# Kernel tuning notes

Hardware: AMD Instinct MI355X
Metric: run time of the kernel (lower is better)

The kernel has to match this reference:

```python
import jax, jax.numpy as jnp
import numpy as np

B, S, D, F_DIM, E, TOP_K = 4, 2048, 1024, 1024, 8, 2


def setup_inputs() -> dict:
    key = jax.random.key(0)
    ks = jax.random.split(key, 6)
    return {
        "x": jax.random.normal(ks[0], (B, S, D), jnp.float32),
        "router_w": jax.random.normal(ks[1], (E, D), jnp.float32) * 0.02,
        "router_b": jax.random.normal(ks[2], (E,), jnp.float32) * 0.02,
        "expert_w": jax.random.normal(ks[3], (E, F_DIM, D), jnp.float32) * 0.02,
        "expert_b": jax.random.normal(ks[4], (E, F_DIM), jnp.float32) * 0.02,
        "expert_pref": jax.random.normal(ks[5], (E, D), jnp.float32),
        "top_k": TOP_K,
    }


def reference(x, router_w, router_b, expert_w, expert_b, expert_pref, top_k):
    num_experts = expert_w.shape[0]
    # Router: softmax over experts, then top-k with renormalization
    logits = jnp.einsum("bsd,ed->bse", x, router_w) + router_b
    routing_weights = jax.nn.softmax(logits, axis=-1)            # [B,S,E]
    top_w, top_idx = jax.lax.top_k(routing_weights, top_k)       # [B,S,K]
    top_w = top_w / jnp.sum(top_w, axis=-1, keepdims=True)
    # Dense per-expert combine weight: sum of renormalized top-k weights routed to each expert
    onehot = jax.nn.one_hot(top_idx, num_experts, dtype=x.dtype)  # [B,S,K,E]
    comb = jnp.einsum("bske,bsk->bse", onehot, top_w)             # [B,S,E]
    # Per-expert linear for every token, weighted combine (dense grouped-GEMM form)
    expert_out = jnp.einsum("bsd,efd->bsef", x, expert_w) + expert_b  # [B,S,E,F]
    final_output = jnp.einsum("bsef,bse->bsf", expert_out, comb)      # [B,S,F]
    # Expert utilization: fraction of tokens whose top-k contains expert i
    mask = jnp.sum(onehot, axis=2) > 0                            # [B,S,E]
    expert_utilization = jnp.mean(mask.astype(x.dtype), axis=(0, 1))
    # Load balance loss: MSE of mean routing weight vs ideal uniform usage
    usage = jnp.mean(routing_weights, axis=(0, 1))
    load_balance_loss = jnp.mean((usage - 1.0 / num_experts) ** 2)
    # Diversity: mean pairwise L2 distance over concatenated expert params (fixed small E)
    flat = jnp.concatenate(
        [expert_w.reshape(num_experts, -1), expert_b, expert_pref], axis=1
    )  # [E, P]
    dists = [jnp.linalg.norm(flat[i] - flat[j])
             for i in range(num_experts) for j in range(i + 1, num_experts)]
    diversity_score = jnp.mean(jnp.stack(dists))
    return final_output, routing_weights, expert_utilization, load_balance_loss, diversity_score
```

## Files before the change

kernel.cpp:

```cpp
#include <hip/hip_runtime.h>
#include <stdint.h>

typedef unsigned short u16;
typedef __attribute__((ext_vector_type(4))) float f32x4;
typedef __attribute__((ext_vector_type(8))) short bf16x8;

#define NTOK 8192
#define DDIM 1024
#define FDIM 1024
#define NEXP 8
#define PCAP 8192
#define RBLK 512

__device__ __align__(256) u16 g_xb[NTOK * DDIM];
__device__ __align__(256) u16 g_wbf[NEXP * FDIM * DDIM];
__device__ __align__(256) float g_buf0[NTOK * FDIM];
__device__ __align__(256) float g_buf1[NTOK * FDIM];
__device__ __align__(256) int g_ptok[NEXP * PCAP];
__device__ __align__(256) float g_pw[NEXP * PCAP];
__device__ __align__(256) unsigned g_e01[NTOK];
__device__ __align__(256) float g_w0[NTOK];
__device__ __align__(256) float g_w1[NTOK];
__device__ __align__(256) float g_usage_part[RBLK * NEXP];
__device__ __align__(256) int g_tile[256];
__device__ int g_ntile;
__device__ int g_cnt[16];
__device__ float g_gram[40];

__device__ __forceinline__ u16 f2bf(float f) {
  unsigned u = __builtin_bit_cast(unsigned, f);
  unsigned r = u + 0x7fffu + ((u >> 16) & 1u);
  return (u16)(r >> 16);
}

__device__ __forceinline__ void gload_lds16(const void* g, void* l) {
  __builtin_amdgcn_global_load_lds(
      (const __attribute__((address_space(1))) void*)g,
      (__attribute__((address_space(3))) void*)l, 16, 0, 0);
}

__global__ __launch_bounds__(64) void k_init() {
  const int tid = threadIdx.x;
  if (tid < 40) g_gram[tid] = 0.f;
}

__global__ __launch_bounds__(256) void k_gram_cast(
    const float* __restrict__ ew, const float* __restrict__ ebias,
    const float* __restrict__ epref) {
  const int P0 = FDIM * DDIM;
  const int PT = P0 + FDIM + DDIM;
  float g[36];
#pragma unroll
  for (int i = 0; i < 36; ++i) g[i] = 0.f;
  for (int k = blockIdx.x * 256 + threadIdx.x; k < PT; k += gridDim.x * 256) {
    float v[8];
    if (k < P0) {
#pragma unroll
      for (int e = 0; e < 8; ++e) v[e] = ew[(size_t)e * P0 + k];
#pragma unroll
      for (int e = 0; e < 8; ++e) g_wbf[(size_t)e * P0 + k] = f2bf(v[e]);
    } else if (k < P0 + FDIM) {
      int kk = k - P0;
#pragma unroll
      for (int e = 0; e < 8; ++e) v[e] = ebias[e * FDIM + kk];
    } else {
      int kk = k - P0 - FDIM;
#pragma unroll
      for (int e = 0; e < 8; ++e) v[e] = epref[e * DDIM + kk];
    }
    int idx = 0;
#pragma unroll
    for (int i = 0; i < 8; ++i)
#pragma unroll
      for (int j = i; j < 8; ++j) {
        g[idx] += v[i] * v[j];
        ++idx;
      }
  }
#pragma unroll
  for (int i = 0; i < 36; ++i) {
    float a = g[i];
#pragma unroll
    for (int s = 32; s; s >>= 1) a += __shfl_xor(a, s);
    g[i] = a;
  }
  __shared__ float gs[4][36];
  const int w = threadIdx.x >> 6, lane = threadIdx.x & 63;
  if (lane == 0) {
#pragma unroll
    for (int i = 0; i < 36; ++i) gs[w][i] = g[i];
  }
  __syncthreads();
  if (threadIdx.x < 36)
    atomicAdd(&g_gram[threadIdx.x], gs[0][threadIdx.x] + gs[1][threadIdx.x] +
                                        gs[2][threadIdx.x] + gs[3][threadIdx.x]);
}

__global__ __launch_bounds__(256) void k_router(
    const float* __restrict__ x, const float* __restrict__ rwg,
    const float* __restrict__ rb, float* __restrict__ rwout) {
  __shared__ __align__(16) float rw_lds[NEXP * DDIM];
  __shared__ float us[NEXP];
  const int tid = threadIdx.x;
  const int w = tid >> 6, lane = tid & 63;
  {
    const float4* src = (const float4*)rwg;
    float4* dst = (float4*)rw_lds;
#pragma unroll
    for (int i = 0; i < 8; ++i) dst[tid + 256 * i] = src[tid + 256 * i];
  }
  if (tid < NEXP) us[tid] = 0.f;
  __syncthreads();

  float rbl[NEXP];
#pragma unroll
  for (int e = 0; e < NEXP; ++e) rbl[e] = rb[e];
  float uw[NEXP];
#pragma unroll
  for (int e = 0; e < NEXP; ++e) uw[e] = 0.f;

  for (int it = 0; it < 4; ++it) {
    const int t = blockIdx.x * 16 + w * 4 + it;
    const float4* xv = (const float4*)(x + (size_t)t * DDIM);
    float4 xv4[4];
#pragma unroll
    for (int j = 0; j < 4; ++j) xv4[j] = xv[lane + 64 * j];
    ushort4* xo = (ushort4*)(g_xb + (size_t)t * DDIM);
#pragma unroll
    for (int j = 0; j < 4; ++j) {
      float4 v = xv4[j];
      ushort4 o;
      o.x = f2bf(v.x); o.y = f2bf(v.y); o.z = f2bf(v.z); o.w = f2bf(v.w);
      xo[lane + 64 * j] = o;
    }
    float lg[NEXP];
#pragma unroll
    for (int e = 0; e < NEXP; ++e) {
      float a = 0.f;
#pragma unroll
      for (int j = 0; j < 4; ++j) {
        float4 r = *(const float4*)&rw_lds[e * DDIM + (lane + 64 * j) * 4];
        float4 v = xv4[j];
        a += v.x * r.x + v.y * r.y + v.z * r.z + v.w * r.w;
      }
      lg[e] = a;
    }
#pragma unroll
    for (int e = 0; e < NEXP; ++e) {
      float a = lg[e];
#pragma unroll
      for (int s = 32; s; s >>= 1) a += __shfl_xor(a, s);
      lg[e] = a + rbl[e];
    }
    float mx = lg[0];
#pragma unroll
    for (int e = 1; e < NEXP; ++e) mx = fmaxf(mx, lg[e]);
    float p[NEXP];
    float sm = 0.f;
#pragma unroll
    for (int e = 0; e < NEXP; ++e) {
      p[e] = expf(lg[e] - mx);
      sm += p[e];
    }
    float inv = 1.f / sm;
#pragma unroll
    for (int e = 0; e < NEXP; ++e) {
      p[e] *= inv;
      uw[e] += p[e];
    }
    int e0 = 0;
    float b0 = p[0];
#pragma unroll
    for (int e = 1; e < NEXP; ++e)
      if (p[e] > b0) { b0 = p[e]; e0 = e; }
    int e1 = -1;
    float b1 = -1.f;
#pragma unroll
    for (int e = 0; e < NEXP; ++e)
      if (e != e0 && p[e] > b1) { b1 = p[e]; e1 = e; }
    if (lane == 0) {
      float4* rw4 = (float4*)(rwout + (size_t)t * NEXP);
      rw4[0] = make_float4(p[0], p[1], p[2], p[3]);
      rw4[1] = make_float4(p[4], p[5], p[6], p[7]);
      float rn = 1.f / (b0 + b1);
      g_e01[t] = (unsigned)e0 | ((unsigned)e1 << 8);
      g_w0[t] = b0 * rn;
      g_w1[t] = b1 * rn;
    }
  }
  if (lane == 0) {
#pragma unroll
    for (int e = 0; e < NEXP; ++e) atomicAdd(&us[e], uw[e]);
  }
  __syncthreads();
  if (tid < NEXP) g_usage_part[blockIdx.x * NEXP + tid] = us[tid];
}

__global__ __launch_bounds__(256) void k_lists() {
  const int e = blockIdx.x;
  const int tid = threadIdx.x;
  const int wv = tid >> 6, lane = tid & 63;
  __shared__ int wcnt[4];
  int base = 0;
  for (int c = 0; c < NTOK / 256; ++c) {
    const int t = c * 256 + tid;
    unsigned rec = g_e01[t];
    int m0 = (int)(rec & 255u) == e;
    int m1 = (int)((rec >> 8) & 255u) == e;
    unsigned long long bal = __ballot(m0 || m1);
    int rank = __popcll(bal & ((1ull << lane) - 1ull));
    if (lane == 0) wcnt[wv] = __popcll(bal);
    __syncthreads();
    int pre = base;
#pragma unroll
    for (int i = 0; i < 4; ++i)
      if (i < wv) pre += wcnt[i];
    int tot = wcnt[0] + wcnt[1] + wcnt[2] + wcnt[3];
    if (m0 || m1) {
      int idx = pre + rank;
      g_ptok[e * PCAP + idx] = (t << 1) | (m1 ? 1 : 0);
      g_pw[e * PCAP + idx] = m1 ? g_w1[t] : g_w0[t];
    }
    base += tot;
    __syncthreads();
  }
  if (tid == 0) g_cnt[e] = base;
}

__global__ __launch_bounds__(64) void k_tiles() {
  if (threadIdx.x == 0) {
    int t = 0;
    for (int e = 0; e < NEXP; ++e) {
      int nt = (g_cnt[e] + 127) >> 7;
      for (int i = 0; i < nt; ++i) g_tile[t++] = (e << 16) | i;
    }
    g_ntile = t;
  }
}

__global__ __launch_bounds__(256) void k_gemm(const float* __restrict__ eb) {
  const int slot = blockIdx.y;
  if (slot >= g_ntile) return;
  const int tl = g_tile[slot];
  const int e = tl >> 16;
  const int count = g_cnt[e];
  const int m0 = (tl & 0xffff) * 128;
  const int n0 = blockIdx.x * 128;

  __shared__ __align__(16) u16 As[2][128 * 64];
  __shared__ __align__(16) u16 Bs[2][128 * 64];

  const int tid = threadIdx.x;
  const int lane = tid & 63;
  const int w = tid >> 6;
  const int wm = w >> 1, wn = w & 1;
  const int col16 = lane & 15, rg = lane >> 4;

  const int* ptok = g_ptok + e * PCAP;

  const u16* srcA[4];
  const u16* srcB[4];
  unsigned soff[4];
#pragma unroll
  for (int c = 0; c < 4; ++c) {
    int o = c * 4096 + tid * 16;
    int row = o >> 7;
    int sl = (o >> 4) & 7;
    int r = m0 + row;
    if (r > count - 1) r = count - 1;
    int tk = (ptok[r] >> 1) & (NTOK - 1);
    srcA[c] = g_xb + (size_t)tk * DDIM + ((sl ^ (row & 7)) << 3);
    srcB[c] = g_wbf + (size_t)e * (FDIM * DDIM) + (size_t)(n0 + row) * DDIM +
              ((sl ^ (row & 7)) << 3);
    soff[c] = (unsigned)o;
  }

#define STAGE(buf, k0)                                                        \
  {                                                                           \
    _Pragma("unroll") for (int c = 0; c < 4; ++c)                             \
        gload_lds16((const char*)(srcA[c] + (k0)), (char*)As[buf] + soff[c]); \
    _Pragma("unroll") for (int c = 0; c < 4; ++c)                             \
        gload_lds16((const char*)(srcB[c] + (k0)), (char*)Bs[buf] + soff[c]); \
  }

  f32x4 acc[4][4];
  const f32x4 zz = {0.f, 0.f, 0.f, 0.f};
#pragma unroll
  for (int i = 0; i < 4; ++i)
#pragma unroll
    for (int j = 0; j < 4; ++j) acc[i][j] = zz;

  STAGE(0, 0);
  STAGE(1, 64);

  const int sxor = col16 & 7;
  for (int kk = 0; kk < 16; ++kk) {
    const int cur = kk & 1;
    if (kk < 15) {
      asm volatile("s_waitcnt vmcnt(8)" ::: "memory");
    } else {
      asm volatile("s_waitcnt vmcnt(0)" ::: "memory");
    }
    __builtin_amdgcn_s_barrier();
    __builtin_amdgcn_sched_barrier(0);

#pragma unroll
    for (int ki = 0; ki < 2; ++ki) {
      bf16x8 af[4], bg[4];
#pragma unroll
      for (int mi = 0; mi < 4; ++mi) {
        int row = wm * 64 + mi * 16 + col16;
        af[mi] = *(const bf16x8*)(As[cur] + row * 64 +
                                  (((ki * 4 + rg) ^ sxor) << 3));
      }
#pragma unroll
      for (int ni = 0; ni < 4; ++ni) {
        int row = wn * 64 + ni * 16 + col16;
        bg[ni] = *(const bf16x8*)(Bs[cur] + row * 64 +
                                  (((ki * 4 + rg) ^ sxor) << 3));
      }
      __builtin_amdgcn_s_setprio(1);
#pragma unroll
      for (int mi = 0; mi < 4; ++mi)
#pragma unroll
        for (int ni = 0; ni < 4; ++ni)
          acc[mi][ni] = __builtin_amdgcn_mfma_f32_16x16x32_bf16(
              af[mi], bg[ni], acc[mi][ni], 0, 0, 0);
      __builtin_amdgcn_s_setprio(0);
    }

    asm volatile("" ::: "memory");
    __builtin_amdgcn_s_barrier();
    asm volatile("" ::: "memory");
    if (kk + 2 < 16) STAGE(cur, (kk + 2) * 64);
  }
#undef STAGE

#pragma unroll
  for (int mi = 0; mi < 4; ++mi) {
#pragma unroll
    for (int j = 0; j < 4; ++j) {
      int r = m0 + wm * 64 + mi * 16 + rg * 4 + j;
      if (r < count) {
        int enc = ptok[r];
        int tk = (enc >> 1) & (NTOK - 1);
        float wgt = g_pw[e * PCAP + r];
        float* dst = (enc & 1 ? g_buf1 : g_buf0) + (size_t)tk * FDIM + n0 +
                     wn * 64 + col16;
        const float* bias = eb + e * FDIM + n0 + wn * 64 + col16;
#pragma unroll
        for (int ni = 0; ni < 4; ++ni)
          dst[ni * 16] = wgt * (acc[mi][ni][j] + bias[ni * 16]);
      }
    }
  }
}

__global__ __launch_bounds__(256) void k_combine(float4* __restrict__ o, int n) {
  const float4* a = (const float4*)g_buf0;
  const float4* b = (const float4*)g_buf1;
  int i = blockIdx.x * 256 + threadIdx.x;
  int stride = gridDim.x * 256;
  for (; i < n; i += stride) {
    float4 va = a[i], vb = b[i];
    o[i] = make_float4(va.x + vb.x, va.y + vb.y, va.z + vb.z, va.w + vb.w);
  }
}

__global__ __launch_bounds__(256) void k_finalize(float* __restrict__ out_util,
                                                  float* __restrict__ out_lbl,
                                                  float* __restrict__ out_div) {
  const int tid = threadIdx.x;
  __shared__ float su[8][33];
  {
    int e = tid & 7, part = tid >> 3;
    float s = 0.f;
    for (int i = part; i < RBLK; i += 32) s += g_usage_part[i * NEXP + e];
    su[e][part] = s;
  }
  __syncthreads();
  if (tid < 8) {
    float s = 0.f;
#pragma unroll
    for (int i = 0; i < 32; ++i) s += su[tid][i];
    su[tid][32] = s;
    out_util[tid] = (float)g_cnt[tid] * (1.f / 8192.f);
  }
  __syncthreads();
  if (tid == 0) {
    float dv = 0.f;
#pragma unroll
    for (int e = 0; e < 8; ++e) {
      float u = su[e][32] * (1.f / 8192.f) - 0.125f;
      dv += u * u;
    }
    out_lbl[0] = dv * 0.125f;
  }
  if (tid < 64) {
    float ds = 0.f;
    if (tid < 28) {
      int c = tid, i = 0;
      while (c >= 7 - i) { c -= 7 - i; ++i; }
      int j = i + 1 + c;
      auto tri = [](int a2, int b2) {
        return a2 * 8 - (a2 * (a2 - 1)) / 2 + (b2 - a2);
      };
      float d2 = g_gram[tri(i, i)] + g_gram[tri(j, j)] - 2.f * g_gram[tri(i, j)];
      ds = sqrtf(fmaxf(d2, 0.f));
    }
#pragma unroll
    for (int s = 16; s; s >>= 1) ds += __shfl_xor(ds, s);
    if (tid == 0) out_div[0] = ds * (1.f / 28.f);
  }
}

extern "C" void kernel_launch(void* const* d_in, const int* in_sizes, int n_in,
                              void* d_out, int out_size, void* d_ws,
                              size_t ws_size, hipStream_t stream) {
  const float* x = (const float*)d_in[0];
  const float* rwg = (const float*)d_in[1];
  const float* rb = (const float*)d_in[2];
  const float* ew = (const float*)d_in[3];
  const float* eb = (const float*)d_in[4];
  const float* ep = (const float*)d_in[5];

  float* out = (float*)d_out;
  float* out_final = out;
  float* out_rw = out + (size_t)NTOK * FDIM;
  float* out_util = out_rw + (size_t)NTOK * NEXP;
  float* out_lbl = out_util + NEXP;
  float* out_div = out_lbl + 1;

  k_init<<<1, 64, 0, stream>>>();
  k_gram_cast<<<512, 256, 0, stream>>>(ew, eb, ep);
  k_router<<<RBLK, 256, 0, stream>>>(x, rwg, rb, out_rw);
  k_lists<<<8, 256, 0, stream>>>();
  k_tiles<<<1, 64, 0, stream>>>();
  k_gemm<<<dim3(8, 136), 256, 0, stream>>>(eb);
  k_combine<<<2048, 256, 0, stream>>>((float4*)out_final, (NTOK * FDIM) / 4);
  k_finalize<<<1, 256, 0, stream>>>(out_util, out_lbl, out_div);
}
```

Measured before the change: 158.2 us.

## Drop tiny launch kernels, fold finalize into combine, use 8-wave GEMM blocks

```diff
diff --git a/kernel.cpp b/kernel.cpp
--- a/kernel.cpp
+++ b/kernel.cpp
@@ -22,10 +22,8 @@
 __device__ __align__(256) float g_w0[NTOK];
 __device__ __align__(256) float g_w1[NTOK];
 __device__ __align__(256) float g_usage_part[RBLK * NEXP];
-__device__ __align__(256) int g_tile[256];
-__device__ int g_ntile;
+__device__ __align__(256) float g_gram_part[512 * 36];
 __device__ int g_cnt[16];
-__device__ float g_gram[40];
 
 __device__ __forceinline__ u16 f2bf(float f) {
   unsigned u = __builtin_bit_cast(unsigned, f);
@@ -37,11 +35,6 @@
   __builtin_amdgcn_global_load_lds(
       (const __attribute__((address_space(1))) void*)g,
       (__attribute__((address_space(3))) void*)l, 16, 0, 0);
-}
-
-__global__ __launch_bounds__(64) void k_init() {
-  const int tid = threadIdx.x;
-  if (tid < 40) g_gram[tid] = 0.f;
 }
 
 __global__ __launch_bounds__(256) void k_gram_cast(
@@ -92,8 +85,9 @@
   }
   __syncthreads();
   if (threadIdx.x < 36)
-    atomicAdd(&g_gram[threadIdx.x], gs[0][threadIdx.x] + gs[1][threadIdx.x] +
-                                        gs[2][threadIdx.x] + gs[3][threadIdx.x]);
+    g_gram_part[blockIdx.x * 36 + threadIdx.x] =
+        gs[0][threadIdx.x] + gs[1][threadIdx.x] + gs[2][threadIdx.x] +
+        gs[3][threadIdx.x];
 }
 
 __global__ __launch_bounds__(256) void k_router(
@@ -227,24 +221,17 @@
   if (tid == 0) g_cnt[e] = base;
 }
 
-__global__ __launch_bounds__(64) void k_tiles() {
-  if (threadIdx.x == 0) {
-    int t = 0;
-    for (int e = 0; e < NEXP; ++e) {
-      int nt = (g_cnt[e] + 127) >> 7;
-      for (int i = 0; i < nt; ++i) g_tile[t++] = (e << 16) | i;
-    }
-    g_ntile = t;
-  }
-}
-
-__global__ __launch_bounds__(256) void k_gemm(const float* __restrict__ eb) {
-  const int slot = blockIdx.y;
-  if (slot >= g_ntile) return;
-  const int tl = g_tile[slot];
-  const int e = tl >> 16;
+__global__ __launch_bounds__(512) void k_gemm(const float* __restrict__ eb) {
+  int s = blockIdx.y;
+  int e = 0;
+  for (; e < NEXP; ++e) {
+    int nt = (g_cnt[e] + 127) >> 7;
+    if (s < nt) break;
+    s -= nt;
+  }
+  if (e == NEXP) return;
   const int count = g_cnt[e];
-  const int m0 = (tl & 0xffff) * 128;
+  const int m0 = s * 128;
   const int n0 = blockIdx.x * 128;
 
   __shared__ __align__(16) u16 As[2][128 * 64];
@@ -253,17 +240,17 @@
   const int tid = threadIdx.x;
   const int lane = tid & 63;
   const int w = tid >> 6;
-  const int wm = w >> 1, wn = w & 1;
+  const int wm = w >> 2, wn = w & 3;
   const int col16 = lane & 15, rg = lane >> 4;
 
   const int* ptok = g_ptok + e * PCAP;
 
-  const u16* srcA[4];
-  const u16* srcB[4];
-  unsigned soff[4];
-#pragma unroll
-  for (int c = 0; c < 4; ++c) {
-    int o = c * 4096 + tid * 16;
+  const u16* srcA[2];
+  const u16* srcB[2];
+  unsigned soff[2];
+#pragma unroll
+  for (int c = 0; c < 2; ++c) {
+    int o = c * 8192 + tid * 16;
     int row = o >> 7;
     int sl = (o >> 4) & 7;
     int r = m0 + row;
@@ -277,18 +264,18 @@
 
 #define STAGE(buf, k0)                                                        \
   {                                                                           \
-    _Pragma("unroll") for (int c = 0; c < 4; ++c)                             \
+    _Pragma("unroll") for (int c = 0; c < 2; ++c)                             \
         gload_lds16((const char*)(srcA[c] + (k0)), (char*)As[buf] + soff[c]); \
-    _Pragma("unroll") for (int c = 0; c < 4; ++c)                             \
+    _Pragma("unroll") for (int c = 0; c < 2; ++c)                             \
         gload_lds16((const char*)(srcB[c] + (k0)), (char*)Bs[buf] + soff[c]); \
   }
 
-  f32x4 acc[4][4];
+  f32x4 acc[4][2];
   const f32x4 zz = {0.f, 0.f, 0.f, 0.f};
 #pragma unroll
   for (int i = 0; i < 4; ++i)
 #pragma unroll
-    for (int j = 0; j < 4; ++j) acc[i][j] = zz;
+    for (int j = 0; j < 2; ++j) acc[i][j] = zz;
 
   STAGE(0, 0);
   STAGE(1, 64);
@@ -297,7 +284,7 @@
   for (int kk = 0; kk < 16; ++kk) {
     const int cur = kk & 1;
     if (kk < 15) {
-      asm volatile("s_waitcnt vmcnt(8)" ::: "memory");
+      asm volatile("s_waitcnt vmcnt(4)" ::: "memory");
     } else {
       asm volatile("s_waitcnt vmcnt(0)" ::: "memory");
     }
@@ -306,7 +293,7 @@
 
 #pragma unroll
     for (int ki = 0; ki < 2; ++ki) {
-      bf16x8 af[4], bg[4];
+      bf16x8 af[4], bg[2];
 #pragma unroll
       for (int mi = 0; mi < 4; ++mi) {
         int row = wm * 64 + mi * 16 + col16;
@@ -314,8 +301,8 @@
                                   (((ki * 4 + rg) ^ sxor) << 3));
       }
 #pragma unroll
-      for (int ni = 0; ni < 4; ++ni) {
-        int row = wn * 64 + ni * 16 + col16;
+      for (int ni = 0; ni < 2; ++ni) {
+        int row = wn * 32 + ni * 16 + col16;
         bg[ni] = *(const bf16x8*)(Bs[cur] + row * 64 +
                                   (((ki * 4 + rg) ^ sxor) << 3));
       }
@@ -323,7 +310,7 @@
 #pragma unroll
       for (int mi = 0; mi < 4; ++mi)
 #pragma unroll
-        for (int ni = 0; ni < 4; ++ni)
+        for (int ni = 0; ni < 2; ++ni)
           acc[mi][ni] = __builtin_amdgcn_mfma_f32_16x16x32_bf16(
               af[mi], bg[ni], acc[mi][ni], 0, 0, 0);
       __builtin_amdgcn_s_setprio(0);
@@ -346,71 +333,79 @@
         int tk = (enc >> 1) & (NTOK - 1);
         float wgt = g_pw[e * PCAP + r];
         float* dst = (enc & 1 ? g_buf1 : g_buf0) + (size_t)tk * FDIM + n0 +
-                     wn * 64 + col16;
-        const float* bias = eb + e * FDIM + n0 + wn * 64 + col16;
-#pragma unroll
-        for (int ni = 0; ni < 4; ++ni)
+                     wn * 32 + col16;
+        const float* bias = eb + e * FDIM + n0 + wn * 32 + col16;
+#pragma unroll
+        for (int ni = 0; ni < 2; ++ni)
           dst[ni * 16] = wgt * (acc[mi][ni][j] + bias[ni * 16]);
       }
     }
   }
 }
 
-__global__ __launch_bounds__(256) void k_combine(float4* __restrict__ o, int n) {
+__global__ __launch_bounds__(256) void k_combine(float4* __restrict__ o, int n,
+                                                 float* __restrict__ out_util,
+                                                 float* __restrict__ out_lbl,
+                                                 float* __restrict__ out_div) {
+  const int tid = threadIdx.x;
+  if (blockIdx.x == 0) {
+    __shared__ float su[8][33];
+    __shared__ float sg[36][5];
+    {
+      int e = tid & 7, part = tid >> 3;
+      float s = 0.f;
+      for (int i = part; i < RBLK; i += 32) s += g_usage_part[i * NEXP + e];
+      su[e][part] = s;
+      int gi = tid >> 2, gp = tid & 3;
+      if (gi < 36) {
+        float gsum = 0.f;
+        for (int i = gp; i < 512; i += 4) gsum += g_gram_part[i * 36 + gi];
+        sg[gi][gp] = gsum;
+      }
+    }
+    __syncthreads();
+    if (tid < 8) {
+      float s2 = 0.f;
+#pragma unroll
+      for (int i = 0; i < 32; ++i) s2 += su[tid][i];
+      su[tid][32] = s2;
+      out_util[tid] = (float)g_cnt[tid] * (1.f / 8192.f);
+    }
+    if (tid < 36) sg[tid][4] = sg[tid][0] + sg[tid][1] + sg[tid][2] + sg[tid][3];
+    __syncthreads();
+    if (tid == 0) {
+      float dv = 0.f;
+#pragma unroll
+      for (int e = 0; e < 8; ++e) {
+        float u = su[e][32] * (1.f / 8192.f) - 0.125f;
+        dv += u * u;
+      }
+      out_lbl[0] = dv * 0.125f;
+    }
+    if (tid < 64) {
+      float ds = 0.f;
+      if (tid < 28) {
+        int c = tid, i = 0;
+        while (c >= 7 - i) { c -= 7 - i; ++i; }
+        int j = i + 1 + c;
+        auto tri = [](int a2, int b2) {
+          return a2 * 8 - (a2 * (a2 - 1)) / 2 + (b2 - a2);
+        };
+        float d2 = sg[tri(i, i)][4] + sg[tri(j, j)][4] - 2.f * sg[tri(i, j)][4];
+        ds = sqrtf(fmaxf(d2, 0.f));
+      }
+#pragma unroll
+      for (int s = 16; s; s >>= 1) ds += __shfl_xor(ds, s);
+      if (tid == 0) out_div[0] = ds * (1.f / 28.f);
+    }
+  }
   const float4* a = (const float4*)g_buf0;
   const float4* b = (const float4*)g_buf1;
-  int i = blockIdx.x * 256 + threadIdx.x;
+  int i = blockIdx.x * 256 + tid;
   int stride = gridDim.x * 256;
   for (; i < n; i += stride) {
     float4 va = a[i], vb = b[i];
     o[i] = make_float4(va.x + vb.x, va.y + vb.y, va.z + vb.z, va.w + vb.w);
-  }
-}
-
-__global__ __launch_bounds__(256) void k_finalize(float* __restrict__ out_util,
-                                                  float* __restrict__ out_lbl,
-                                                  float* __restrict__ out_div) {
-  const int tid = threadIdx.x;
-  __shared__ float su[8][33];
-  {
-    int e = tid & 7, part = tid >> 3;
-    float s = 0.f;
-    for (int i = part; i < RBLK; i += 32) s += g_usage_part[i * NEXP + e];
-    su[e][part] = s;
-  }
-  __syncthreads();
-  if (tid < 8) {
-    float s = 0.f;
-#pragma unroll
-    for (int i = 0; i < 32; ++i) s += su[tid][i];
-    su[tid][32] = s;
-    out_util[tid] = (float)g_cnt[tid] * (1.f / 8192.f);
-  }
-  __syncthreads();
-  if (tid == 0) {
-    float dv = 0.f;
-#pragma unroll
-    for (int e = 0; e < 8; ++e) {
-      float u = su[e][32] * (1.f / 8192.f) - 0.125f;
-      dv += u * u;
-    }
-    out_lbl[0] = dv * 0.125f;
-  }
-  if (tid < 64) {
-    float ds = 0.f;
-    if (tid < 28) {
-      int c = tid, i = 0;
-      while (c >= 7 - i) { c -= 7 - i; ++i; }
-      int j = i + 1 + c;
-      auto tri = [](int a2, int b2) {
-        return a2 * 8 - (a2 * (a2 - 1)) / 2 + (b2 - a2);
-      };
-      float d2 = g_gram[tri(i, i)] + g_gram[tri(j, j)] - 2.f * g_gram[tri(i, j)];
-      ds = sqrtf(fmaxf(d2, 0.f));
-    }
-#pragma unroll
-    for (int s = 16; s; s >>= 1) ds += __shfl_xor(ds, s);
-    if (tid == 0) out_div[0] = ds * (1.f / 28.f);
   }
 }
 
@@ -431,12 +426,10 @@
   float* out_lbl = out_util + NEXP;
   float* out_div = out_lbl + 1;
 
-  k_init<<<1, 64, 0, stream>>>();
   k_gram_cast<<<512, 256, 0, stream>>>(ew, eb, ep);
   k_router<<<RBLK, 256, 0, stream>>>(x, rwg, rb, out_rw);
   k_lists<<<8, 256, 0, stream>>>();
-  k_tiles<<<1, 64, 0, stream>>>();
-  k_gemm<<<dim3(8, 136), 256, 0, stream>>>(eb);
-  k_combine<<<2048, 256, 0, stream>>>((float4*)out_final, (NTOK * FDIM) / 4);
-  k_finalize<<<1, 256, 0, stream>>>(out_util, out_lbl, out_div);
-}
+  k_gemm<<<dim3(8, 136), 512, 0, stream>>>(eb);
+  k_combine<<<2048, 256, 0, stream>>>((float4*)out_final, (NTOK * FDIM) / 4,
+                                      out_util, out_lbl, out_div);
+}
```

After: 166.9 us. 5.6% more time.
